# Kernel tuning notes

Hardware: AMD Instinct MI355X
Metric: run time of the kernel (lower is better)

## Reference

```python
import jax, jax.numpy as jnp
import numpy as np

B, C, H, W = 4, 256, 64, 64
DQK = C // 4


def setup_inputs() -> dict:
    key = jax.random.key(0)
    ks = jax.random.split(key, 5)
    s = 0.05
    x = jax.random.normal(ks[0], (B, C, H, W), dtype=jnp.float32)
    Wq = jax.random.normal(ks[1], (DQK, C), dtype=jnp.float32) * s
    Wk = jax.random.normal(ks[2], (DQK, C), dtype=jnp.float32) * s
    Wv = jax.random.normal(ks[3], (C, C), dtype=jnp.float32) * s
    bq = jnp.zeros((DQK,), jnp.float32)
    bk = jnp.zeros((DQK,), jnp.float32)
    bv = jnp.zeros((C,), jnp.float32)
    gamma = jnp.zeros((1,), jnp.float32)
    return {"x": x, "Wq": Wq, "bq": bq, "Wk": Wk, "bk": bk,
            "Wv": Wv, "bv": bv, "gamma": gamma}


def reference(x, Wq, bq, Wk, bk, Wv, bv, gamma):
    b, c, h, w = x.shape
    n = h * w
    xf = x.reshape(b, c, n)                      # [B, C, N]
    # 1x1 convs == per-pixel linear projections
    q = jnp.einsum('dc,bcn->bnd', Wq, xf) + bq   # [B, N, Dqk]
    k = jnp.einsum('dc,bcn->bdn', Wk, xf) + bk[None, :, None]  # [B, Dqk, N]
    v = jnp.einsum('ec,bcn->ben', Wv, xf) + bv[None, :, None]  # [B, C, N]
    energy = jnp.einsum('bnd,bdm->bnm', q, k)    # [B, N, N]
    attn = jax.nn.softmax(energy, axis=-1)       # softmax over keys
    # out[b,c,i] = sum_j v[b,c,j] * attn[b,i,j]
    out = jnp.einsum('bcj,bij->bci', v, attn)    # [B, C, N]
    out = out.reshape(b, c, h, w)
    return gamma * out + x
```

## Files before the change

### kernel.cpp

```cpp
#include <hip/hip_runtime.h>

#define B_ 4
#define C_ 256
#define N_ 4096
#define D_ 64

typedef __bf16 bf16x8 __attribute__((ext_vector_type(8)));
typedef float floatx4 __attribute__((ext_vector_type(4)));
typedef unsigned short ushort8v __attribute__((ext_vector_type(8)));
typedef unsigned short ushort4v __attribute__((ext_vector_type(4)));
typedef unsigned short ushort2v __attribute__((ext_vector_type(2)));

static __device__ __forceinline__ unsigned short f2bf(float f) {
    unsigned int u = __builtin_bit_cast(unsigned int, f);
    u += 0x7fffu + ((u >> 16) & 1u);
    return (unsigned short)(u >> 16);
}
static __device__ __forceinline__ float bf2f(unsigned short h) {
    unsigned int u = ((unsigned int)h) << 16;
    return __builtin_bit_cast(float, u);
}

#define GLOAD16(gp, lp)                                                      \
    __builtin_amdgcn_global_load_lds(                                        \
        (const __attribute__((address_space(1))) void*)(gp),                 \
        (__attribute__((address_space(3))) void*)(lp), 16, 0, 0)

__global__ __launch_bounds__(256) void convert_w(
    const float* __restrict__ Wq, const float* __restrict__ Wk,
    const float* __restrict__ Wv, unsigned short* __restrict__ WbfA)
{
    int tid = blockIdx.x * 256 + threadIdx.x;
    int p0  = tid * 4;
    int j0   = p0 & 7;
    int lane = (p0 >> 3) & 63;
    int sidx = p0 >> 9;
    int ft = sidx >> 3, ks = sidx & 7;
    int m  = lane & 15, g = lane >> 4;
    int f  = 16*ft + m;
    int c  = 32*ks + 8*g + j0;
    const float* src = (f < 64)  ? (Wq + (size_t)f * C_)
                     : (f < 128) ? (Wk + (size_t)(f - 64) * C_)
                                 : (Wv + (size_t)(f - 128) * C_);
    float4 v = *(const float4*)(src + c);
    ushort4v u;
    u[0] = f2bf(v.x); u[1] = f2bf(v.y); u[2] = f2bf(v.z); u[3] = f2bf(v.w);
    *(ushort4v*)(WbfA + p0) = u;
}

__global__ __launch_bounds__(256, 3) void proj_kernel(
    const float* __restrict__ x, const unsigned short* __restrict__ WbfA,
    const float* __restrict__ bq, const float* __restrict__ bk,
    const float* __restrict__ bv,
    unsigned short* __restrict__ Qg, unsigned short* __restrict__ Kg,
    unsigned short* __restrict__ Vg)
{
    __shared__ __align__(16) unsigned short smem[64 * 264];
    unsigned short* xs = smem;
    unsigned short* Lt = smem;

    const int n0 = blockIdx.x * 64;
    const int f0 = blockIdx.y * 128;
    const int b  = blockIdx.z;
    const int t  = threadIdx.x;
    const int w  = t >> 6;
    const int lane = t & 63;
    const int g  = lane >> 4;
    const int m  = lane & 15;

#pragma unroll
    for (int k = 0; k < 8; ++k) {
        int e  = t + 256 * k;
        int cp = e >> 4;
        int c  = 2 * cp;
        int n4 = (e & 15) * 4;
        float4 v0 = *(const float4*)(x + ((size_t)b*C_ + c    )*N_ + n0 + n4);
        float4 v1 = *(const float4*)(x + ((size_t)b*C_ + c + 1)*N_ + n0 + n4);
        float a0[4] = {v0.x, v0.y, v0.z, v0.w};
        float a1[4] = {v1.x, v1.y, v1.z, v1.w};
#pragma unroll
        for (int j = 0; j < 4; ++j) {
            int n = n4 + j;
            ushort2v u2;
            u2[0] = f2bf(a0[j]);
            u2[1] = f2bf(a1[j]);
            *(ushort2v*)&xs[n*264 + (((c >> 3) ^ (n & 7)) << 3) + (c & 7)] = u2;
        }
    }

    float bias_[2][4];
#pragma unroll
    for (int mt = 0; mt < 2; ++mt)
#pragma unroll
        for (int r = 0; r < 4; ++r) {
            int fg = f0 + 32*w + 16*mt + 4*g + r;
            bias_[mt][r] = (fg < 64) ? bq[fg]
                         : (fg < 128) ? bk[fg - 64] : bv[fg - 128];
        }

    const unsigned short* Wa0 = WbfA + (size_t)(((f0 >> 4) + 2*w    )*8)*512
                              + lane*8;
    const unsigned short* Wa1 = WbfA + (size_t)(((f0 >> 4) + 2*w + 1)*8)*512
                              + lane*8;

    floatx4 acc[2][4];
#pragma unroll
    for (int mt = 0; mt < 2; ++mt)
#pragma unroll
        for (int nt = 0; nt < 4; ++nt) acc[mt][nt] = (floatx4){0.f,0.f,0.f,0.f};

    __syncthreads();

#pragma unroll
    for (int ks = 0; ks < 8; ++ks) {
        bf16x8 af[2];
        af[0] = *(const bf16x8*)(Wa0 + ks*512);
        af[1] = *(const bf16x8*)(Wa1 + ks*512);
#pragma unroll
        for (int nt = 0; nt < 4; ++nt) {
            int n = 16*nt + m;
            bf16x8 bfr = *(const bf16x8*)
                &xs[n*264 + (((4*ks + g) ^ (n & 7)) << 3)];
#pragma unroll
            for (int mt = 0; mt < 2; ++mt)
                acc[mt][nt] = __builtin_amdgcn_mfma_f32_16x16x32_bf16(
                                  af[mt], bfr, acc[mt][nt], 0, 0, 0);
        }
    }

    __syncthreads();

#pragma unroll
    for (int mt = 0; mt < 2; ++mt)
#pragma unroll
        for (int nt = 0; nt < 4; ++nt)
#pragma unroll
            for (int r = 0; r < 4; ++r)
                Lt[(32*w + 16*mt + 4*g + r)*72 + 16*nt + m] =
                    f2bf(acc[mt][nt][r] + bias_[mt][r]);
    __syncthreads();

    if (f0 == 0) {
#pragma unroll
        for (int k = 0; k < 4; ++k) {
            int e   = t + 256 * k;
            int fq0 = (e >> 6) * 8;
            int nl  = e & 63;
            ushort8v u;
#pragma unroll
            for (int j = 0; j < 8; ++j) u[j] = Lt[(fq0 + j)*72 + nl];
            unsigned short* dst = (fq0 < 64)
                ? (Qg + ((size_t)b*N_ + n0 + nl)*D_ + fq0)
                : (Kg + ((size_t)b*N_ + n0 + nl)*D_ + (fq0 - 64));
            *(ushort8v*)dst = u;
        }
    } else {
        const int cb = f0 - 128;
#pragma unroll
        for (int k = 0; k < 4; ++k) {
            int e  = t + 256 * k;
            int fr = e >> 3;
            int n8 = (e & 7) * 8;
            ushort8v u = *(const ushort8v*)&Lt[fr*72 + n8];
            *(ushort8v*)(Vg + ((size_t)b*C_ + cb + fr)*N_ + n0 + n8) = u;
        }
    }
}

__global__ __launch_bounds__(512, 2) void flash_kernel(
    const unsigned short* __restrict__ Qg, const unsigned short* __restrict__ Kg,
    const unsigned short* __restrict__ Vg,
    unsigned short* __restrict__ Opart, float* __restrict__ ML)
{
    __shared__ __align__(16) unsigned short Vlds[32 * 512];
    __shared__ __align__(16) unsigned short Klds[2][8 * 512];
    __shared__ __align__(16) unsigned short PA[16 * 64 * 8];
    __shared__ float AL[128];

    const int g8   = blockIdx.x;
    const int tile = blockIdx.y;
    const int half = g8 & 1;
    const int b    = g8 >> 1;
    const int n0   = tile * 128;
    const int t    = threadIdx.x;
    const int w    = t >> 6;
    const int lane = t & 63;
    const int g    = lane >> 4;
    const int m    = lane & 15;
    const int wq   = w >> 2;
    const int cq   = w & 3;

    const unsigned short* Qb = Qg + ((size_t)b*N_ + n0)*D_;
    const unsigned short* Kb = Kg + (size_t)b*N_*D_;
    const unsigned short* Vb = Vg + (size_t)b*C_*N_;

    const int cstart = half * 32;
    const int cend   = cstart + 32;

    bf16x8 qf[2];
#pragma unroll
    for (int ks = 0; ks < 2; ++ks)
        qf[ks] = *(const bf16x8*)(Qb + (size_t)(16*w + m)*D_ + 32*ks + 8*g);

    floatx4 accO[4][4];
#pragma unroll
    for (int rt = 0; rt < 4; ++rt)
#pragma unroll
        for (int ct = 0; ct < 4; ++ct)
            accO[rt][ct] = (floatx4){0.f, 0.f, 0.f, 0.f};

    float mrow = -1e30f, lrow = 0.f;

    {
        const unsigned short* gp =
            Kb + (size_t)(cstart*64 + 16*(w >> 1) + m)*D_ + 32*(w & 1) + 8*g;
        GLOAD16(gp, &Klds[0][w * 512]);
    }
    __syncthreads();

    for (int t64 = cstart; t64 < cend; ++t64) {
        const int j0 = t64 * 64;
        const int kb = (t64 - cstart) & 1;

#pragma unroll
        for (int u = 0; u < 4; ++u) {
            int sidx = 4*w + u;
            int ks   = sidx >> 4;
            int cb   = sidx & 15;
            const unsigned short* gp =
                Vb + (size_t)(16*cb + m)*N_ + j0 + 32*ks + 8*g;
            GLOAD16(gp, &Vlds[sidx * 512]);
        }
        if (t64 + 1 < cend) {
            const unsigned short* gp =
                Kb + (size_t)((t64+1)*64 + 16*(w >> 1) + m)*D_
                   + 32*(w & 1) + 8*g;
            GLOAD16(gp, &Klds[kb ^ 1][w * 512]);
        }

        floatx4 accST[4];
#pragma unroll
        for (int jt = 0; jt < 4; ++jt) accST[jt] = (floatx4){0.f,0.f,0.f,0.f};
#pragma unroll
        for (int ks = 0; ks < 2; ++ks)
#pragma unroll
            for (int jt = 0; jt < 4; ++jt) {
                bf16x8 kfr = *(const bf16x8*)
                    &Klds[kb][(jt*2 + ks)*512 + lane*8];
                accST[jt] = __builtin_amdgcn_mfma_f32_16x16x32_bf16(
                                kfr, qf[ks], accST[jt], 0, 0, 0);
            }

        float mx = -1e30f;
#pragma unroll
        for (int jt = 0; jt < 4; ++jt)
#pragma unroll
            for (int r = 0; r < 4; ++r) mx = fmaxf(mx, accST[jt][r]);
        mx = fmaxf(mx, __shfl_xor(mx, 16));
        mx = fmaxf(mx, __shfl_xor(mx, 32));
        float mnew  = fmaxf(mrow, mx);
        float alpha = __expf(mrow - mnew);
        mrow = mnew;
        float p[4][4];
        float rs = 0.f;
#pragma unroll
        for (int jt = 0; jt < 4; ++jt)
#pragma unroll
            for (int r = 0; r < 4; ++r) {
                float e = __expf(accST[jt][r] - mnew);
                p[jt][r] = e;
                rs += e;
            }
        rs += __shfl_xor(rs, 16);
        rs += __shfl_xor(rs, 32);
        lrow = lrow * alpha + rs;

        if (g == 0) AL[16*w + m] = alpha;

#pragma unroll
        for (int jt = 0; jt < 4; ++jt) {
            ushort4v u;
#pragma unroll
            for (int r = 0; r < 4; ++r) u[r] = f2bf(p[jt][r]);
            int frag = (w*2 + (jt >> 1))*64 + 16*(2*(jt & 1) + (g >> 1)) + m;
            *(ushort4v*)&PA[frag*8 + 4*(g & 1)] = u;
        }

        __syncthreads();

#pragma unroll
        for (int rt = 0; rt < 4; ++rt) {
            floatx4 a4 = *(const floatx4*)&AL[64*wq + 16*rt + 4*g];
#pragma unroll
            for (int ct = 0; ct < 4; ++ct)
                accO[rt][ct] *= a4;
        }
#pragma unroll
        for (int ks = 0; ks < 2; ++ks) {
            bf16x8 pf[4];
#pragma unroll
            for (int rt = 0; rt < 4; ++rt)
                pf[rt] = *(const bf16x8*)
                    &PA[((8*wq + rt*2 + ks)*64 + lane)*8];
#pragma unroll
            for (int ct = 0; ct < 4; ++ct) {
                int sidx = ks*16 + 4*cq + ct;
                bf16x8 vfrag = *(const bf16x8*)&Vlds[sidx*512 + lane*8];
#pragma unroll
                for (int rt = 0; rt < 4; ++rt)
                    accO[rt][ct] = __builtin_amdgcn_mfma_f32_16x16x32_bf16(
                                       pf[rt], vfrag, accO[rt][ct], 0, 0, 0);
            }
        }

        __syncthreads();
    }

    const size_t tbase = ((size_t)(half*B_ + b)*32 + tile);
    unsigned short* Ob = Opart + tbase * (C_ * 128);
    float* ml = ML + tbase * 256;

    if (g == 0) {
        ml[16*w + m]       = mrow;
        ml[128 + 16*w + m] = lrow;
    }

#pragma unroll
    for (int rt = 0; rt < 4; ++rt)
#pragma unroll
        for (int ct = 0; ct < 4; ++ct) {
            int c  = 64*cq + 16*ct + m;
            int q0 = 64*wq + 16*rt + 4*g;
            ushort4v u4;
#pragma unroll
            for (int r = 0; r < 4; ++r) u4[r] = f2bf(accO[rt][ct][r]);
            *(ushort4v*)(Ob + (size_t)c*128 + q0) = u4;
        }
}

__global__ __launch_bounds__(256) void combine_kernel(
    const unsigned short* __restrict__ Opart, const float* __restrict__ ML,
    const float* __restrict__ x, const float* __restrict__ gamma,
    float* __restrict__ out)
{
    __shared__ float sc0[128], sc1[128];
    const int tile  = blockIdx.x;
    const int chalf = blockIdx.y;
    const int b     = blockIdx.z;
    const int n0    = tile * 128;
    const int t     = threadIdx.x;

    if (t < 128) {
        const float* ml0 = ML + ((size_t)(0*B_ + b)*32 + tile)*256;
        const float* ml1 = ML + ((size_t)(1*B_ + b)*32 + tile)*256;
        float m0 = ml0[t], l0 = ml0[128 + t];
        float m1 = ml1[t], l1 = ml1[128 + t];
        float M  = fmaxf(m0, m1);
        float f0 = __expf(m0 - M), f1 = __expf(m1 - M);
        float L  = f0*l0 + f1*l1;
        float gm = gamma[0];
        sc0[t] = gm * f0 / L;
        sc1[t] = gm * f1 / L;
    }
    __syncthreads();

    const int nq = t & 31;
    const int cl = t >> 5;
    const float* xb = x   + (size_t)b*C_*N_;
    float*       ob = out + (size_t)b*C_*N_;
    const unsigned short* O0 = Opart + ((size_t)(0*B_ + b)*32 + tile)*(C_*128);
    const unsigned short* O1 = Opart + ((size_t)(1*B_ + b)*32 + tile)*(C_*128);

    float s0[4], s1[4];
#pragma unroll
    for (int k = 0; k < 4; ++k) { s0[k] = sc0[4*nq + k]; s1[k] = sc1[4*nq + k]; }

#pragma unroll 4
    for (int i = 0; i < 16; ++i) {
        int c = 128*chalf + 8*i + cl;
        float4 x4 = *(const float4*)(xb + (size_t)c*N_ + n0 + 4*nq);
        ushort4v a4 = *(const ushort4v*)(O0 + (size_t)c*128 + 4*nq);
        ushort4v b4 = *(const ushort4v*)(O1 + (size_t)c*128 + 4*nq);
        float4 y;
        y.x = s0[0]*bf2f(a4[0]) + s1[0]*bf2f(b4[0]) + x4.x;
        y.y = s0[1]*bf2f(a4[1]) + s1[1]*bf2f(b4[1]) + x4.y;
        y.z = s0[2]*bf2f(a4[2]) + s1[2]*bf2f(b4[2]) + x4.z;
        y.w = s0[3]*bf2f(a4[3]) + s1[3]*bf2f(b4[3]) + x4.w;
        *(float4*)(ob + (size_t)c*N_ + n0 + 4*nq) = y;
    }
}

extern "C" void kernel_launch(void* const* d_in, const int* in_sizes, int n_in,
                              void* d_out, int out_size, void* d_ws, size_t ws_size,
                              hipStream_t stream) {
    const float* x     = (const float*)d_in[0];
    const float* Wq    = (const float*)d_in[1];
    const float* bq    = (const float*)d_in[2];
    const float* Wk    = (const float*)d_in[3];
    const float* bk    = (const float*)d_in[4];
    const float* Wv    = (const float*)d_in[5];
    const float* bv    = (const float*)d_in[6];
    const float* gamma = (const float*)d_in[7];
    float* out = (float*)d_out;

    unsigned short* Qg = (unsigned short*)d_ws;
    unsigned short* Kg = Qg + (size_t)B_*N_*D_;
    unsigned short* Vg = Kg + (size_t)B_*N_*D_;
    unsigned short* Op = Vg + (size_t)B_*C_*N_;
    float* ML = (float*)(Op + (size_t)2*B_*32*C_*128);
    unsigned short* WbfA = (unsigned short*)(ML + (size_t)2*B_*32*256);

    convert_w<<<dim3(96), 256, 0, stream>>>(Wq, Wk, Wv, WbfA);
    proj_kernel<<<dim3(64, 3, 4), 256, 0, stream>>>(x, WbfA, bq, bk, bv,
                                                    Qg, Kg, Vg);
    flash_kernel<<<dim3(8, 32), 512, 0, stream>>>(Qg, Kg, Vg, Op, ML);
    combine_kernel<<<dim3(32, 2, 4), 256, 0, stream>>>(Op, ML, x, gamma, out);
}
```

Measured before the change: 179.4 us.

## Split flash attention keys into four partitions and raise occupancy

The key dimension is split four ways instead of two, so the flash kernel launches 512 blocks instead of 256. This fills more CUs on the MI355X's 256 CUs. Launch bounds are raised to 4 blocks per CU, and the MFMA section gets a higher wave priority via s_setprio. The combine kernel now merges four partial outputs with log-sum-exp rescaling. In exchange it doubles the partial-output workspace traffic and adds register pressure from the tighter launch bounds.

```diff
diff --git a/kernel.cpp b/kernel.cpp
--- a/kernel.cpp
+++ b/kernel.cpp
@@ -167,7 +167,7 @@
     }
 }
 
-__global__ __launch_bounds__(512, 2) void flash_kernel(
+__global__ __launch_bounds__(512, 4) void flash_kernel(
     const unsigned short* __restrict__ Qg, const unsigned short* __restrict__ Kg,
     const unsigned short* __restrict__ Vg,
     unsigned short* __restrict__ Opart, float* __restrict__ ML)
@@ -177,10 +177,10 @@
     __shared__ __align__(16) unsigned short PA[16 * 64 * 8];
     __shared__ float AL[128];
 
-    const int g8   = blockIdx.x;
+    const int gx   = blockIdx.x;
     const int tile = blockIdx.y;
-    const int half = g8 & 1;
-    const int b    = g8 >> 1;
+    const int quarter = gx & 3;
+    const int b    = gx >> 2;
     const int n0   = tile * 128;
     const int t    = threadIdx.x;
     const int w    = t >> 6;
@@ -194,8 +194,8 @@
     const unsigned short* Kb = Kg + (size_t)b*N_*D_;
     const unsigned short* Vb = Vg + (size_t)b*C_*N_;
 
-    const int cstart = half * 32;
-    const int cend   = cstart + 32;
+    const int cstart = quarter * 16;
+    const int cend   = cstart + 16;
 
     bf16x8 qf[2];
 #pragma unroll
@@ -295,6 +295,7 @@
             for (int ct = 0; ct < 4; ++ct)
                 accO[rt][ct] *= a4;
         }
+        __builtin_amdgcn_s_setprio(1);
 #pragma unroll
         for (int ks = 0; ks < 2; ++ks) {
             bf16x8 pf[4];
@@ -312,11 +313,12 @@
                                        pf[rt], vfrag, accO[rt][ct], 0, 0, 0);
             }
         }
+        __builtin_amdgcn_s_setprio(0);
 
         __syncthreads();
     }
 
-    const size_t tbase = ((size_t)(half*B_ + b)*32 + tile);
+    const size_t tbase = ((size_t)(quarter*B_ + b)*32 + tile);
     unsigned short* Ob = Opart + tbase * (C_ * 128);
     float* ml = ML + tbase * 256;
 
@@ -343,7 +345,7 @@
     const float* __restrict__ x, const float* __restrict__ gamma,
     float* __restrict__ out)
 {
-    __shared__ float sc0[128], sc1[128];
+    __shared__ float sc[4][128];
     const int tile  = blockIdx.x;
     const int chalf = blockIdx.y;
     const int b     = blockIdx.z;
@@ -351,16 +353,22 @@
     const int t     = threadIdx.x;
 
     if (t < 128) {
-        const float* ml0 = ML + ((size_t)(0*B_ + b)*32 + tile)*256;
-        const float* ml1 = ML + ((size_t)(1*B_ + b)*32 + tile)*256;
-        float m0 = ml0[t], l0 = ml0[128 + t];
-        float m1 = ml1[t], l1 = ml1[128 + t];
-        float M  = fmaxf(m0, m1);
-        float f0 = __expf(m0 - M), f1 = __expf(m1 - M);
-        float L  = f0*l0 + f1*l1;
+        float mm[4], ll[4];
+        float M = -1e30f;
+#pragma unroll
+        for (int s = 0; s < 4; ++s) {
+            const float* mls = ML + ((size_t)(s*B_ + b)*32 + tile)*256;
+            mm[s] = mls[t];
+            ll[s] = mls[128 + t];
+            M = fmaxf(M, mm[s]);
+        }
+        float fs[4];
+        float L = 0.f;
+#pragma unroll
+        for (int s = 0; s < 4; ++s) { fs[s] = __expf(mm[s] - M); L += fs[s]*ll[s]; }
         float gm = gamma[0];
-        sc0[t] = gm * f0 / L;
-        sc1[t] = gm * f1 / L;
+#pragma unroll
+        for (int s = 0; s < 4; ++s) sc[s][t] = gm * fs[s] / L;
     }
     __syncthreads();
 
@@ -368,24 +376,30 @@
     const int cl = t >> 5;
     const float* xb = x   + (size_t)b*C_*N_;
     float*       ob = out + (size_t)b*C_*N_;
-    const unsigned short* O0 = Opart + ((size_t)(0*B_ + b)*32 + tile)*(C_*128);
-    const unsigned short* O1 = Opart + ((size_t)(1*B_ + b)*32 + tile)*(C_*128);
-
-    float s0[4], s1[4];
-#pragma unroll
-    for (int k = 0; k < 4; ++k) { s0[k] = sc0[4*nq + k]; s1[k] = sc1[4*nq + k]; }
+    const unsigned short* Os[4];
+#pragma unroll
+    for (int s = 0; s < 4; ++s)
+        Os[s] = Opart + ((size_t)(s*B_ + b)*32 + tile)*(C_*128);
+
+    float sv[4][4];
+#pragma unroll
+    for (int s = 0; s < 4; ++s)
+#pragma unroll
+        for (int k = 0; k < 4; ++k) sv[s][k] = sc[s][4*nq + k];
 
 #pragma unroll 4
     for (int i = 0; i < 16; ++i) {
         int c = 128*chalf + 8*i + cl;
         float4 x4 = *(const float4*)(xb + (size_t)c*N_ + n0 + 4*nq);
-        ushort4v a4 = *(const ushort4v*)(O0 + (size_t)c*128 + 4*nq);
-        ushort4v b4 = *(const ushort4v*)(O1 + (size_t)c*128 + 4*nq);
-        float4 y;
-        y.x = s0[0]*bf2f(a4[0]) + s1[0]*bf2f(b4[0]) + x4.x;
-        y.y = s0[1]*bf2f(a4[1]) + s1[1]*bf2f(b4[1]) + x4.y;
-        y.z = s0[2]*bf2f(a4[2]) + s1[2]*bf2f(b4[2]) + x4.z;
-        y.w = s0[3]*bf2f(a4[3]) + s1[3]*bf2f(b4[3]) + x4.w;
+        float4 y = x4;
+#pragma unroll
+        for (int s = 0; s < 4; ++s) {
+            ushort4v a4 = *(const ushort4v*)(Os[s] + (size_t)c*128 + 4*nq);
+            y.x += sv[s][0]*bf2f(a4[0]);
+            y.y += sv[s][1]*bf2f(a4[1]);
+            y.z += sv[s][2]*bf2f(a4[2]);
+            y.w += sv[s][3]*bf2f(a4[3]);
+        }
         *(float4*)(ob + (size_t)c*N_ + n0 + 4*nq) = y;
     }
 }
@@ -407,12 +421,12 @@
     unsigned short* Kg = Qg + (size_t)B_*N_*D_;
     unsigned short* Vg = Kg + (size_t)B_*N_*D_;
     unsigned short* Op = Vg + (size_t)B_*C_*N_;
-    float* ML = (float*)(Op + (size_t)2*B_*32*C_*128);
-    unsigned short* WbfA = (unsigned short*)(ML + (size_t)2*B_*32*256);
+    float* ML = (float*)(Op + (size_t)4*B_*32*C_*128);
+    unsigned short* WbfA = (unsigned short*)(ML + (size_t)4*B_*32*256);
 
     convert_w<<<dim3(96), 256, 0, stream>>>(Wq, Wk, Wv, WbfA);
     proj_kernel<<<dim3(64, 3, 4), 256, 0, stream>>>(x, WbfA, bq, bk, bv,
                                                     Qg, Kg, Vg);
-    flash_kernel<<<dim3(8, 32), 512, 0, stream>>>(Qg, Kg, Vg, Op, ML);
+    flash_kernel<<<dim3(16, 32), 512, 0, stream>>>(Qg, Kg, Vg, Op, ML);
     combine_kernel<<<dim3(32, 2, 4), 256, 0, stream>>>(Op, ML, x, gamma, out);
 }
```

After: 198.9 us. 10.9% more time.

## Software-pipeline flash loop: overlap previous tile's PV with current QK and softmax

Applied to the files above, without the earlier changes.

Double-buffers the V tile, the P scratch and the alpha rescale array so each iteration can run the P·V MFMAs for the previous key tile while the current tile's QK^T and softmax proceed. This cuts the loop to one barrier per iteration and adds a final drain step after the loop. PV MFMAs are wrapped in raised wave priority via s_setprio. LDS use grows from about 64 KB to about 113 KB per block, which may stop two 512-thread blocks from sharing a CU despite the launch bounds.

```diff
diff --git a/kernel.cpp b/kernel.cpp
--- a/kernel.cpp
+++ b/kernel.cpp
@@ -172,10 +172,10 @@
     const unsigned short* __restrict__ Vg,
     unsigned short* __restrict__ Opart, float* __restrict__ ML)
 {
-    __shared__ __align__(16) unsigned short Vlds[32 * 512];
+    __shared__ __align__(16) unsigned short Vlds[2][32 * 512];
     __shared__ __align__(16) unsigned short Klds[2][8 * 512];
-    __shared__ __align__(16) unsigned short PA[16 * 64 * 8];
-    __shared__ float AL[128];
+    __shared__ __align__(16) unsigned short PA[2][16 * 64 * 8];
+    __shared__ float AL[2][128];
 
     const int g8   = blockIdx.x;
     const int tile = blockIdx.y;
@@ -216,11 +216,12 @@
             Kb + (size_t)(cstart*64 + 16*(w >> 1) + m)*D_ + 32*(w & 1) + 8*g;
         GLOAD16(gp, &Klds[0][w * 512]);
     }
-    __syncthreads();
 
     for (int t64 = cstart; t64 < cend; ++t64) {
-        const int j0 = t64 * 64;
-        const int kb = (t64 - cstart) & 1;
+        const int cur = t64 & 1;
+        const int j0  = t64 * 64;
+
+        __syncthreads();
 
 #pragma unroll
         for (int u = 0; u < 4; ++u) {
@@ -229,13 +230,13 @@
             int cb   = sidx & 15;
             const unsigned short* gp =
                 Vb + (size_t)(16*cb + m)*N_ + j0 + 32*ks + 8*g;
-            GLOAD16(gp, &Vlds[sidx * 512]);
+            GLOAD16(gp, &Vlds[cur][sidx * 512]);
         }
         if (t64 + 1 < cend) {
             const unsigned short* gp =
                 Kb + (size_t)((t64+1)*64 + 16*(w >> 1) + m)*D_
                    + 32*(w & 1) + 8*g;
-            GLOAD16(gp, &Klds[kb ^ 1][w * 512]);
+            GLOAD16(gp, &Klds[cur ^ 1][w * 512]);
         }
 
         floatx4 accST[4];
@@ -246,10 +247,41 @@
 #pragma unroll
             for (int jt = 0; jt < 4; ++jt) {
                 bf16x8 kfr = *(const bf16x8*)
-                    &Klds[kb][(jt*2 + ks)*512 + lane*8];
+                    &Klds[cur][(jt*2 + ks)*512 + lane*8];
                 accST[jt] = __builtin_amdgcn_mfma_f32_16x16x32_bf16(
                                 kfr, qf[ks], accST[jt], 0, 0, 0);
             }
+
+        if (t64 > cstart) {
+#pragma unroll
+            for (int rt = 0; rt < 4; ++rt) {
+                floatx4 a4 = *(const floatx4*)
+                    &AL[cur ^ 1][64*wq + 16*rt + 4*g];
+#pragma unroll
+                for (int ct = 0; ct < 4; ++ct)
+                    accO[rt][ct] *= a4;
+            }
+            __builtin_amdgcn_s_setprio(1);
+#pragma unroll
+            for (int ks = 0; ks < 2; ++ks) {
+                bf16x8 pf[4];
+#pragma unroll
+                for (int rt = 0; rt < 4; ++rt)
+                    pf[rt] = *(const bf16x8*)
+                        &PA[cur ^ 1][((8*wq + rt*2 + ks)*64 + lane)*8];
+#pragma unroll
+                for (int ct = 0; ct < 4; ++ct) {
+                    int sidx = ks*16 + 4*cq + ct;
+                    bf16x8 vfrag = *(const bf16x8*)
+                        &Vlds[cur ^ 1][sidx*512 + lane*8];
+#pragma unroll
+                    for (int rt = 0; rt < 4; ++rt)
+                        accO[rt][ct] = __builtin_amdgcn_mfma_f32_16x16x32_bf16(
+                                           pf[rt], vfrag, accO[rt][ct], 0, 0, 0);
+                }
+            }
+            __builtin_amdgcn_s_setprio(0);
+        }
 
         float mx = -1e30f;
 #pragma unroll
@@ -275,7 +307,7 @@
         rs += __shfl_xor(rs, 32);
         lrow = lrow * alpha + rs;
 
-        if (g == 0) AL[16*w + m] = alpha;
+        if (g == 0) AL[cur][16*w + m] = alpha;
 
 #pragma unroll
         for (int jt = 0; jt < 4; ++jt) {
@@ -283,14 +315,17 @@
 #pragma unroll
             for (int r = 0; r < 4; ++r) u[r] = f2bf(p[jt][r]);
             int frag = (w*2 + (jt >> 1))*64 + 16*(2*(jt & 1) + (g >> 1)) + m;
-            *(ushort4v*)&PA[frag*8 + 4*(g & 1)] = u;
-        }
-
-        __syncthreads();
-
+            *(ushort4v*)&PA[cur][frag*8 + 4*(g & 1)] = u;
+        }
+    }
+
+    __syncthreads();
+
+    {
+        const int cur = (cend - 1) & 1;
 #pragma unroll
         for (int rt = 0; rt < 4; ++rt) {
-            floatx4 a4 = *(const floatx4*)&AL[64*wq + 16*rt + 4*g];
+            floatx4 a4 = *(const floatx4*)&AL[cur][64*wq + 16*rt + 4*g];
 #pragma unroll
             for (int ct = 0; ct < 4; ++ct)
                 accO[rt][ct] *= a4;
@@ -301,19 +336,18 @@
 #pragma unroll
             for (int rt = 0; rt < 4; ++rt)
                 pf[rt] = *(const bf16x8*)
-                    &PA[((8*wq + rt*2 + ks)*64 + lane)*8];
+                    &PA[cur][((8*wq + rt*2 + ks)*64 + lane)*8];
 #pragma unroll
             for (int ct = 0; ct < 4; ++ct) {
                 int sidx = ks*16 + 4*cq + ct;
-                bf16x8 vfrag = *(const bf16x8*)&Vlds[sidx*512 + lane*8];
+                bf16x8 vfrag = *(const bf16x8*)
+                    &Vlds[cur][sidx*512 + lane*8];
 #pragma unroll
                 for (int rt = 0; rt < 4; ++rt)
                     accO[rt][ct] = __builtin_amdgcn_mfma_f32_16x16x32_bf16(
                                        pf[rt], vfrag, accO[rt][ct], 0, 0, 0);
             }
         }
-
-        __syncthreads();
     }
 
     const size_t tbase = ((size_t)(half*B_ + b)*32 + tile);
```

New measurement: 191.8 us. 1.07x slower.
